# Optimization experiments

Measured on AMD Instinct MI355X. Metric: run time of the kernel, lower is better.

## Reference

```python
import jax, jax.numpy as jnp
import numpy as np

E = 256   # embed_size
H = 256   # hidden_size
C = 3     # channels
V = 257   # pixel vocab (0..255 + boundary token 256)
B, R, CO = 128, 32, 32


def setup_inputs() -> dict:
    key = jax.random.key(0)
    ks = jax.random.split(key, 16)
    s = 0.05
    return {
        "x": jax.random.randint(ks[0], (B, C, R, CO), 0, V),
        "emb": jax.random.normal(ks[1], (C, V, E), dtype=jnp.float32) * s,
        "xcomb_W": jax.random.normal(ks[2], (C, E, 2 * E), dtype=jnp.float32) * s,
        "xcomb_b": jax.random.normal(ks[3], (C, E), dtype=jnp.float32) * s,
        "hcomb_W": jax.random.normal(ks[4], (C, H, 2 * H), dtype=jnp.float32) * s,
        "hcomb_b": jax.random.normal(ks[5], (C, H), dtype=jnp.float32) * s,
        "W_ih": jax.random.normal(ks[6], (C, 3 * H, E + 2), dtype=jnp.float32) * s,
        "W_hh": jax.random.normal(ks[7], (C, 3 * H, H), dtype=jnp.float32) * s,
        "b_ih": jax.random.normal(ks[8], (C, 3 * H), dtype=jnp.float32) * s,
        "b_hh": jax.random.normal(ks[9], (C, 3 * H), dtype=jnp.float32) * s,
        "red_W": jax.random.normal(ks[10], (V, H), dtype=jnp.float32) * s,
        "red_b": jax.random.normal(ks[11], (V,), dtype=jnp.float32) * s,
        "green_W": jax.random.normal(ks[12], (V, H + E), dtype=jnp.float32) * s,
        "green_b": jax.random.normal(ks[13], (V,), dtype=jnp.float32) * s,
        "blue_W": jax.random.normal(ks[14], (V, H + 2 * E), dtype=jnp.float32) * s,
        "blue_b": jax.random.normal(ks[15], (V,), dtype=jnp.float32) * s,
    }


def _forward(x, emb, xcomb_W, xcomb_b, hcomb_W, hcomb_b, W_ih, W_hh, b_ih, b_hh,
             red_W, red_b, green_W, green_b, blue_W, blue_b):
    Bb, Cc, Rr, Co = x.shape
    Nr, Nc = Rr - 1, Co - 1
    Hd = W_hh.shape[-1]
    dt = emb.dtype

    # context pixel indices for each output position (row+1,col+1)
    left = x[:, :, 1:, :-1]    # x[:,c,row+1,col]
    above = x[:, :, :-1, 1:]   # x[:,c,row,col+1]
    target = x[:, :, 1:, 1:]   # x[:,c,row+1,col+1] (conditioning embeds for green/blue)

    # per-channel embedding gather, vectorized over all positions
    gather = jax.vmap(lambda t, idx: t[idx], in_axes=(0, 1), out_axes=1)
    left_e = gather(emb, left)      # [B,C,Nr,Nc,E]
    above_e = gather(emb, above)
    target_e = gather(emb, target)

    # x_comb linear on cat(left,above); hidden-independent -> precompute
    xi = jnp.concatenate([left_e, above_e], axis=-1)                     # [B,C,Nr,Nc,2E]
    xi = jnp.einsum('bcrke,cfe->bcrkf', xi, xcomb_W) + xcomb_b[None, :, None, None, :]

    # positional (row,col) features appended as floats (torch.cat promotion)
    pos_r = jnp.broadcast_to(jnp.arange(Nr, dtype=dt)[:, None], (Nr, Nc))
    pos_c = jnp.broadcast_to(jnp.arange(Nc, dtype=dt)[None, :], (Nr, Nc))
    pos = jnp.broadcast_to(jnp.stack([pos_r, pos_c], -1)[None, None], (Bb, Cc, Nr, Nc, 2))
    xfull = jnp.concatenate([xi, pos], axis=-1)                          # [B,C,Nr,Nc,E+2]

    # GRU input projection is hidden-independent -> precompute gates_x
    gx = jnp.einsum('bcrkf,cgf->bcrkg', xfull, W_ih) + b_ih[None, :, None, None, :]
    gx = jnp.transpose(gx, (2, 3, 1, 0, 4))                              # [Nr,Nc,C,B,3H]

    def col_step(prev_left, xs):
        gx_col, prev_row_col = xs   # [C,B,3H], [C,B,H]
        pl = prev_left              # [B,H], shared across channels and cols
        hs = []
        for c in range(Cc):         # fixed small channel loop (sequential dependence)
            hcat = jnp.concatenate([pl, prev_row_col[c]], axis=-1)       # [B,2H]
            h = hcat @ hcomb_W[c].T + hcomb_b[c]                          # [B,H]
            gh = h @ W_hh[c].T + b_hh[c]                                  # [B,3H]
            gxr, gxz, gxn = jnp.split(gx_col[c], 3, axis=-1)
            ghr, ghz, ghn = jnp.split(gh, 3, axis=-1)
            r = jax.nn.sigmoid(gxr + ghr)
            z = jax.nn.sigmoid(gxz + ghz)
            n = jnp.tanh(gxn + r * ghn)
            hnew = (1.0 - z) * n + z * h
            pl = hnew
            hs.append(hnew)
        return pl, jnp.stack(hs, 0)  # carry, [C,B,H]

    def row_step(prev_row, gx_row):
        # prev_row: hiddens from previous row [Nc,C,B,H]
        init_left = jnp.zeros((Bb, Hd), dtype=dt)
        _, hs_row = jax.lax.scan(col_step, init_left, (gx_row, prev_row))
        return hs_row, hs_row

    init_row = jnp.zeros((Nc, Cc, Bb, Hd), dtype=dt)
    _, h_all = jax.lax.scan(row_step, init_row, gx)   # [Nr,Nc,C,B,H]

    te = jnp.transpose(target_e, (2, 3, 1, 0, 4))     # [Nr,Nc,C,B,E]
    h0, h1, h2 = h_all[:, :, 0], h_all[:, :, 1], h_all[:, :, 2]  # [Nr,Nc,B,H]
    lr = h0 @ red_W.T + red_b
    lg = jnp.concatenate([h1, te[:, :, 0]], -1) @ green_W.T + green_b
    lb = jnp.concatenate([h2, te[:, :, 0], te[:, :, 1]], -1) @ blue_W.T + blue_b
    logits = jnp.stack([lr, lg, lb], 0)               # [C,Nr,Nc,B,V]
    return jnp.transpose(logits, (3, 0, 1, 2, 4))     # [B,C,Nr,Nc,V]


def reference(x, emb, xcomb_W, xcomb_b, hcomb_W, hcomb_b, W_ih, W_hh, b_ih, b_hh,
              red_W, red_b, green_W, green_b, blue_W, blue_b):
    return _forward(x, emb, xcomb_W, xcomb_b, hcomb_W, hcomb_b, W_ih, W_hh,
                    b_ih, b_hh, red_W, red_b, green_W, green_b, blue_W, blue_b)
```

## Files before the change

### kernel.cpp

```cpp
#include <hip/hip_runtime.h>

typedef __attribute__((ext_vector_type(4))) float f32x4;
typedef __attribute__((ext_vector_type(8))) short s16x8;
typedef unsigned long long u64;

__device__ __forceinline__ unsigned short f2bf(float f) {
  union { float f; unsigned u; } v; v.f = f;
  unsigned r = v.u + 0x7fffu + ((v.u >> 16) & 1u);
  return (unsigned short)(r >> 16);
}


__global__ void prep_wbig(const float* __restrict__ hcomb_W, const float* __restrict__ hcomb_b,
                          const float* __restrict__ W_hh, const float* __restrict__ b_hh,
                          unsigned short* __restrict__ Wbig, float* __restrict__ bbig) {
  __shared__ float red[256];
  const int c = blockIdx.x, g = blockIdx.y, t = threadIdx.x;
  const float* hW = hcomb_W + (size_t)c * 256 * 512;
  unsigned short* orow = Wbig + ((size_t)c * 1024 + g) * 512;
  if (g < 256) {
    orow[t]       = f2bf(hW[(size_t)g * 512 + t]);
    orow[t + 256] = f2bf(hW[(size_t)g * 512 + t + 256]);
    if (t == 0) bbig[c * 1024 + g] = hcomb_b[c * 256 + g];
    return;
  }
  const int gp = g - 256;
  const float* wrow = W_hh + ((size_t)c * 768 + gp) * 256;
  float a0 = 0.f, a1 = 0.f;
  for (int h = 0; h < 256; h++) {
    float w = wrow[h];
    a0 += w * hW[(size_t)h * 512 + t];
    a1 += w * hW[(size_t)h * 512 + t + 256];
  }
  orow[t] = f2bf(a0); orow[t + 256] = f2bf(a1);
  red[t] = wrow[t] * hcomb_b[c * 256 + t];
  __syncthreads();
  for (int s = 128; s > 0; s >>= 1) { if (t < s) red[t] += red[t + s]; __syncthreads(); }
  if (t == 0) bbig[c * 1024 + g] = red[0] + b_hh[c * 768 + gp];
}

__global__ void prep_u(const float* __restrict__ emb, const float* __restrict__ xcomb_W,
                       float* __restrict__ Ul, float* __restrict__ Ua) {
  __shared__ float er[256];
  const int c = blockIdx.x, v = blockIdx.y, side = blockIdx.z, f = threadIdx.x;
  er[f] = emb[((size_t)c * 257 + v) * 256 + f];
  __syncthreads();
  const float* wrow = xcomb_W + ((size_t)c * 256 + f) * 512 + side * 256;
  float a = 0.f;
  for (int e = 0; e < 256; e++) a += er[e] * wrow[e];
  (side ? Ua : Ul)[((size_t)c * 257 + v) * 256 + f] = a;
}

__global__ void prep_t(const float* __restrict__ W_ih, const float* __restrict__ Ul,
                       const float* __restrict__ Ua, float* __restrict__ Tl, float* __restrict__ Ta) {
  __shared__ float ur[256];
  const int c = blockIdx.x, v = blockIdx.y, side = blockIdx.z, g = threadIdx.x;
  if (g < 256) ur[g] = (side ? Ua : Ul)[((size_t)c * 257 + v) * 256 + g];
  __syncthreads();
  const float* wrow = W_ih + ((size_t)c * 768 + g) * 258;
  float a = 0.f;
  for (int f = 0; f < 256; f++) a += ur[f] * wrow[f];
  (side ? Ta : Tl)[((size_t)c * 257 + v) * 768 + g] = a;
}

__global__ void prep_bgx(const float* __restrict__ W_ih, const float* __restrict__ xcomb_b,
                         const float* __restrict__ b_ih, float* __restrict__ bgx) {
  __shared__ float xb[256];
  const int c = blockIdx.x, g = threadIdx.x;
  if (g < 256) xb[g] = xcomb_b[c * 256 + g];
  __syncthreads();
  const float* wrow = W_ih + ((size_t)c * 768 + g) * 258;
  float a = b_ih[c * 768 + g];
  for (int f = 0; f < 256; f++) a += xb[f] * wrow[f];
  bgx[c * 768 + g] = a;
}

__global__ void prep_tgb(const float* __restrict__ emb, const float* __restrict__ green_W,
                         const float* __restrict__ blue_W,
                         float* __restrict__ TG, float* __restrict__ TB0, float* __restrict__ TB1) {
  __shared__ float er[256];
  const int v = blockIdx.x, which = blockIdx.y, u = threadIdx.x;
  const int ch = (which == 2) ? 1 : 0;
  if (u < 256) er[u] = emb[((size_t)ch * 257 + v) * 256 + u];
  __syncthreads();
  if (u >= 257) return;
  const float* W; int pitch, off; float* T;
  if (which == 0)      { W = green_W; pitch = 512; off = 256; T = TG;  }
  else if (which == 1) { W = blue_W;  pitch = 768; off = 256; T = TB0; }
  else                 { W = blue_W;  pitch = 768; off = 512; T = TB1; }
  const float* wrow = W + (size_t)u * pitch + off;
  float a = 0.f;
  for (int e = 0; e < 256; e++) a += er[e] * wrow[e];
  T[(size_t)v * 257 + u] = a;
}

__global__ void prep_w3(const float* __restrict__ red_W, const float* __restrict__ green_W,
                        const float* __restrict__ blue_W, unsigned short* __restrict__ W3) {
  const int c = blockIdx.x, v = blockIdx.y, t = threadIdx.x;
  float val = 0.f;
  if (v < 257) {
    if (c == 0)      val = red_W[(size_t)v * 256 + t];
    else if (c == 1) val = green_W[(size_t)v * 512 + t];
    else             val = blue_W[(size_t)v * 768 + t];
  }
  W3[((size_t)c * 272 + v) * 256 + t] = f2bf(val);
}

__global__ void prep_gx(const int* __restrict__ x,
                        const float* __restrict__ Tl, const float* __restrict__ Ta,
                        const float* __restrict__ bgx, const float* __restrict__ bbig,
                        const float* __restrict__ W_ih, float* __restrict__ pregx) {
  __shared__ float base[768];
  __shared__ int ix0[128], ix1[128];
  const int r = blockIdx.x, k = blockIdx.y, c = blockIdx.z, tid = threadIdx.x;
  for (int g = tid; g < 768; g += 256) {
    float v = bgx[c * 768 + g]
            + (float)r * W_ih[((size_t)c * 768 + g) * 258 + 256]
            + (float)k * W_ih[((size_t)c * 768 + g) * 258 + 257];
    if (g < 512) v += bbig[c * 1024 + 256 + g];
    base[g] = v;
  }
  if (tid < 128) {
    ix0[tid] = x[((tid * 3 + c) * 32 + (r + 1)) * 32 + k];
    ix1[tid] = x[((tid * 3 + c) * 32 + r) * 32 + (k + 1)];
  }
  __syncthreads();
  const size_t cell = ((size_t)(r * 31 + k)) * 3 + c;
  float* outp = pregx + cell * 3 * 128 * 256;
  const float* Tlc = Tl + (size_t)c * 257 * 768;
  const float* Tac = Ta + (size_t)c * 257 * 768;
  #pragma unroll 2
  for (int b = 0; b < 128; ++b) {
    const float* tl = Tlc + (size_t)ix0[b] * 768;
    const float* ta = Tac + (size_t)ix1[b] * 768;
    #pragma unroll
    for (int q = 0; q < 3; ++q) {
      const int g = q * 256 + tid;
      outp[((size_t)q * 128 + b) * 256 + tid] = tl[g] + ta[g] + base[g];
    }
  }
}

__global__ void zero_flags(int* __restrict__ f, int n) {
  int i = blockIdx.x * 256 + threadIdx.x;
  if (i < n) f[i] = 0;
}


__device__ __forceinline__ void spinwait(int* f, int target) {
  while (__hip_atomic_load(f, __ATOMIC_RELAXED, __HIP_MEMORY_SCOPE_AGENT) < target)
    __builtin_amdgcn_s_sleep(2);
}

__global__ __launch_bounds__(256, 2)
void persist_kernel(const int* __restrict__ x, float* __restrict__ hbuf,
                    const unsigned short* __restrict__ Wbig, const float* __restrict__ bbig,
                    const float* __restrict__ pregx,
                    const unsigned short* __restrict__ W3,
                    const float* __restrict__ TG, const float* __restrict__ TB0,
                    const float* __restrict__ TB1,
                    const float* __restrict__ red_b, const float* __restrict__ green_b,
                    const float* __restrict__ blue_b,
                    float* __restrict__ out, int* __restrict__ flags)
{
  __shared__ unsigned short Abuf[128 * 136];
  __shared__ int idx0[128], idx1[128];

  const int id = blockIdx.x;
  const int rlo = id & 7, slot = id >> 3;
  const int rhi = slot / 5, role = slot - 5 * rhi;
  const int r = rlo + 8 * rhi;
  if (r > 30) return;

  int* sflag = flags;
  int* eflag = flags + 124 * 31;

  const int tid = threadIdx.x;
  const int lane = tid & 63, wv = tid >> 6;
  const int quad = lane >> 4, l16 = lane & 15;

  if (role < 4) {
    const int jcol = role * 64 + wv * 16;
    const int j = jcol + l16;

    for (int L = r; L <= r + 92; ++L) {
      const int t = L - r;
      const int k = t / 3, c = t - 3 * k;
      const size_t cell = ((size_t)(r * 31 + k)) * 3 + c;
      const float* pg = pregx + cell * 3 * 128 * 256;

      f32x4 acc[8][4];
      const float bh  = bbig[c * 1024 + j];
      const float bn3 = bbig[c * 1024 + 768 + j];
      #pragma unroll
      for (int mt = 0; mt < 8; ++mt)
        #pragma unroll
        for (int i = 0; i < 4; ++i) {
          const int b = mt * 16 + quad * 4 + i;
          acc[mt][0][i] = bh;
          acc[mt][1][i] = pg[(size_t)b * 256 + j];
          acc[mt][2][i] = pg[(size_t)(128 + b) * 256 + j];
          acc[mt][3][i] = bn3;
        }

      if (tid == 0) {
        if (t >= 1) spinwait(&sflag[(L - 1) * 31 + r], 4);
        if (r >= 1) spinwait(&sflag[(L - 1) * 31 + (r - 1)], 4);
        if (t >= 3) {
          if (r < 30) spinwait(&sflag[(L - 2) * 31 + (r + 1)], 4);
          spinwait(&eflag[(L - 2) * 31 + r], 1);
        }
      }
      __syncthreads();
      __builtin_amdgcn_fence(__ATOMIC_ACQUIRE, "agent");

      const bool pl_zero = (t == 0);
      const bool a_zero  = (r == 0);
      const float* plp = hbuf + ((size_t)(r * 3 + (c == 0 ? 2 : c - 1)) * 128) * 256;
      const float* ap  = (r > 0) ? hbuf + ((size_t)((r - 1) * 3 + c) * 128) * 256 : hbuf;
      const unsigned short* Wb = Wbig + (size_t)c * 1024 * 512;

      for (int kc = 0; kc < 4; ++kc) {
        const bool from_pl = (kc < 2);
        const float* src = from_pl ? plp : ap;
        const bool zero = from_pl ? pl_zero : a_zero;
        const int colbase = from_pl ? kc * 128 : (kc - 2) * 128;
        __syncthreads();
        #pragma unroll 8
        for (int it = 0; it < 16; ++it) {
          const int li = it * 256 + tid;
          const int row = li >> 5;
          const int col = (li & 31) * 4;
          unsigned short o0 = 0, o1 = 0, o2 = 0, o3 = 0;
          if (!zero) {
            const float4 v = *(const float4*)(src + (size_t)row * 256 + colbase + col);
            o0 = f2bf(v.x); o1 = f2bf(v.y); o2 = f2bf(v.z); o3 = f2bf(v.w);
          }
          unsigned short* d = &Abuf[row * 136 + col];
          d[0] = o0; d[1] = o1; d[2] = o2; d[3] = o3;
        }
        __syncthreads();
        #pragma unroll
        for (int ks = 0; ks < 4; ++ks) {
          const int kofs = ks * 32 + quad * 8;
          s16x8 bf[4];
          #pragma unroll
          for (int g = 0; g < 4; ++g)
            bf[g] = *(const s16x8*)(Wb + (size_t)(g * 256 + jcol + l16) * 512 + kc * 128 + kofs);
          #pragma unroll
          for (int mt = 0; mt < 8; ++mt) {
            const s16x8 af = *(const s16x8*)&Abuf[(mt * 16 + l16) * 136 + kofs];
            #pragma unroll
            for (int g = 0; g < 4; ++g)
              acc[mt][g] = __builtin_amdgcn_mfma_f32_16x16x32_bf16(af, bf[g], acc[mt][g], 0, 0, 0);
          }
        }
      }

      const float* pgn = pg + (size_t)2 * 128 * 256;
      float* hout = hbuf + ((size_t)(r * 3 + c) * 128) * 256;
      #pragma unroll
      for (int mt = 0; mt < 8; ++mt)
        #pragma unroll
        for (int i = 0; i < 4; ++i) {
          const int b = mt * 16 + quad * 4 + i;
          const float gxn = pgn[(size_t)b * 256 + j];
          const float h  = acc[mt][0][i];
          const float rg = __fdividef(1.f, 1.f + __expf(-acc[mt][1][i]));
          const float zg = __fdividef(1.f, 1.f + __expf(-acc[mt][2][i]));
          const float ng = 1.f - __fdividef(2.f, __expf(2.f * (gxn + rg * acc[mt][3][i])) + 1.f);
          hout[(size_t)b * 256 + j] = (1.f - zg) * ng + zg * h;
        }

      __syncthreads();
      if (tid == 0)
        __hip_atomic_fetch_add(&sflag[L * 31 + r], 1, __ATOMIC_RELEASE, __HIP_MEMORY_SCOPE_AGENT);
    }
  } else {
    for (int Le = r + 1; Le <= r + 93; ++Le) {
      const int t = Le - 1 - r;
      const int k = t / 3, c = t - 3 * k;

      if (tid == 0) spinwait(&sflag[(Le - 1) * 31 + r], 4);
      __syncthreads();
      __builtin_amdgcn_fence(__ATOMIC_ACQUIRE, "agent");

      if (tid < 128) {
        idx0[tid] = x[((tid * 3 + 0) * 32 + (r + 1)) * 32 + (k + 1)];
        idx1[tid] = x[((tid * 3 + 1) * 32 + (r + 1)) * 32 + (k + 1)];
      }

      const float* hsrc = hbuf + ((size_t)(r * 3 + c) * 128) * 256;
      const unsigned short* W3c = W3 + (size_t)c * 272 * 256;

      f32x4 acc[2][17];
      #pragma unroll
      for (int m2 = 0; m2 < 2; ++m2)
        #pragma unroll
        for (int nt = 0; nt < 17; ++nt)
          #pragma unroll
          for (int e = 0; e < 4; ++e) acc[m2][nt][e] = 0.f;

      for (int kc = 0; kc < 2; ++kc) {
        __syncthreads();
        #pragma unroll 8
        for (int it = 0; it < 16; ++it) {
          const int li = it * 256 + tid;
          const int row = li >> 5;
          const int col = (li & 31) * 4;
          const float4 v = *(const float4*)(hsrc + (size_t)row * 256 + kc * 128 + col);
          unsigned short* d = &Abuf[row * 136 + col];
          d[0] = f2bf(v.x); d[1] = f2bf(v.y); d[2] = f2bf(v.z); d[3] = f2bf(v.w);
        }
        __syncthreads();
        if (kc == 1 && tid == 0)
          __hip_atomic_fetch_add(&eflag[Le * 31 + r], 1, __ATOMIC_RELEASE, __HIP_MEMORY_SCOPE_AGENT);
        #pragma unroll
        for (int ks = 0; ks < 4; ++ks) {
          const int kofs = ks * 32 + quad * 8;
          s16x8 af[2];
          #pragma unroll
          for (int m2 = 0; m2 < 2; ++m2)
            af[m2] = *(const s16x8*)&Abuf[((wv * 2 + m2) * 16 + l16) * 136 + kofs];
          #pragma unroll
          for (int nt = 0; nt < 17; ++nt) {
            const s16x8 bf = *(const s16x8*)(W3c + (size_t)(nt * 16 + l16) * 256 + kc * 128 + kofs);
            #pragma unroll
            for (int m2 = 0; m2 < 2; ++m2)
              acc[m2][nt] = __builtin_amdgcn_mfma_f32_16x16x32_bf16(af[m2], bf, acc[m2][nt], 0, 0, 0);
          }
        }
      }

      const float* bias = (c == 0) ? red_b : (c == 1) ? green_b : blue_b;
      #pragma unroll
      for (int m2 = 0; m2 < 2; ++m2)
        #pragma unroll
        for (int i = 0; i < 4; ++i) {
          const int b = (m2 + wv * 2) * 16 + quad * 4 + i;
          const int t0 = idx0[b], t1 = idx1[b];
          float* orow = out + ((size_t)((b * 3 + c) * 31 + r) * 31 + k) * 257;
          #pragma unroll
          for (int nt = 0; nt < 17; ++nt) {
            const int v = nt * 16 + l16;
            if (v < 257) {
              float val = acc[m2][nt][i] + bias[v];
              if (c == 1)      val += TG[(size_t)t0 * 257 + v];
              else if (c == 2) val += TB0[(size_t)t0 * 257 + v] + TB1[(size_t)t1 * 257 + v];
              orow[v] = val;
            }
          }
        }
    }
  }
}


extern "C" void kernel_launch(void* const* d_in, const int* in_sizes, int n_in,
                              void* d_out, int out_size, void* d_ws, size_t ws_size,
                              hipStream_t stream) {
  const int*   x       = (const int*)  d_in[0];
  const float* emb     = (const float*)d_in[1];
  const float* xcomb_W = (const float*)d_in[2];
  const float* xcomb_b = (const float*)d_in[3];
  const float* hcomb_W = (const float*)d_in[4];
  const float* hcomb_b = (const float*)d_in[5];
  const float* W_ih    = (const float*)d_in[6];
  const float* W_hh    = (const float*)d_in[7];
  const float* b_ih    = (const float*)d_in[8];
  const float* b_hh    = (const float*)d_in[9];
  const float* red_W   = (const float*)d_in[10];
  const float* red_b   = (const float*)d_in[11];
  const float* green_W = (const float*)d_in[12];
  const float* green_b = (const float*)d_in[13];
  const float* blue_W  = (const float*)d_in[14];
  const float* blue_b  = (const float*)d_in[15];
  float* out = (float*)d_out;

  char* p = (char*)d_ws;
  auto alloc = [&](size_t bytes) -> char* {
    char* r = p; p += (bytes + 255) & ~(size_t)255; return r;
  };
  float* hbuf          = (float*)alloc((size_t)31 * 3 * 128 * 256 * 4);
  unsigned short* Wbig = (unsigned short*)alloc((size_t)3 * 1024 * 512 * 2);
  float* bbig          = (float*)alloc((size_t)3 * 1024 * 4);
  float* Tl            = (float*)alloc((size_t)3 * 257 * 768 * 4);
  float* Ta            = (float*)alloc((size_t)3 * 257 * 768 * 4);
  float* Ul            = (float*)alloc((size_t)3 * 257 * 256 * 4);
  float* Ua            = (float*)alloc((size_t)3 * 257 * 256 * 4);
  float* bgx           = (float*)alloc((size_t)3 * 768 * 4);
  unsigned short* W3   = (unsigned short*)alloc((size_t)3 * 272 * 256 * 2);
  float* TG            = (float*)alloc((size_t)257 * 257 * 4);
  float* TB0           = (float*)alloc((size_t)257 * 257 * 4);
  float* TB1           = (float*)alloc((size_t)257 * 257 * 4);
  int*   flags         = (int*)  alloc((size_t)2 * 124 * 31 * 4);
  float* pregx         = (float*)alloc((size_t)2883 * 3 * 128 * 256 * 4);

  prep_wbig<<<dim3(3, 1024), dim3(256), 0, stream>>>(hcomb_W, hcomb_b, W_hh, b_hh, Wbig, bbig);
  prep_u<<<dim3(3, 257, 2), dim3(256), 0, stream>>>(emb, xcomb_W, Ul, Ua);
  prep_t<<<dim3(3, 257, 2), dim3(768), 0, stream>>>(W_ih, Ul, Ua, Tl, Ta);
  prep_bgx<<<dim3(3), dim3(768), 0, stream>>>(W_ih, xcomb_b, b_ih, bgx);
  prep_tgb<<<dim3(257, 3), dim3(320), 0, stream>>>(emb, green_W, blue_W, TG, TB0, TB1);
  prep_w3<<<dim3(3, 272), dim3(256), 0, stream>>>(red_W, green_W, blue_W, W3);
  prep_gx<<<dim3(31, 31, 3), dim3(256), 0, stream>>>(x, Tl, Ta, bgx, bbig, W_ih, pregx);
  zero_flags<<<dim3(31), dim3(256), 0, stream>>>(flags, 2 * 124 * 31);

  persist_kernel<<<dim3(160), dim3(256), 0, stream>>>(
      x, hbuf, Wbig, bbig, pregx, W3, TG, TB0, TB1, red_b, green_b, blue_b, out, flags);
}
```

Measured before the change: 10.39 ms.

## Restructure persistent GRU kernel: one 1024-thread block per row, bf16 hidden state, fused gx

Each wavefront row now runs in a single 1024-thread block instead of four 256-thread blocks split by column. This removes the cross-block split of the recurrent GEMM, and the per-step flags need only one arrival instead of four. The precomputed combined W_hh·hcomb weight is replaced by two chained bf16 GEMMs (hcomb, then W_hh) done in double-buffered swizzled LDS. The large pregx precompute buffer is dropped, and the gate inputs are gathered from the Tl/Ta tables inside the step. Hidden state is stored as bf16 with coherent atomic loads and stores, and the logits kernel runs as 31 1024-thread blocks. The trade-off is more matmul work per step and fewer, larger blocks on the serial critical path, in exchange for cutting the large gx memory traffic and some synchronisation.

```diff
diff --git a/kernel.cpp b/kernel.cpp
--- a/kernel.cpp
+++ b/kernel.cpp
@@ -3,40 +3,26 @@
 typedef __attribute__((ext_vector_type(4))) float f32x4;
 typedef __attribute__((ext_vector_type(8))) short s16x8;
 typedef unsigned long long u64;
-
-__device__ __forceinline__ unsigned short f2bf(float f) {
+typedef unsigned short u16;
+
+__device__ __forceinline__ u16 f2bf(float f) {
   union { float f; unsigned u; } v; v.f = f;
   unsigned r = v.u + 0x7fffu + ((v.u >> 16) & 1u);
-  return (unsigned short)(r >> 16);
-}
-
-
-__global__ void prep_wbig(const float* __restrict__ hcomb_W, const float* __restrict__ hcomb_b,
-                          const float* __restrict__ W_hh, const float* __restrict__ b_hh,
-                          unsigned short* __restrict__ Wbig, float* __restrict__ bbig) {
-  __shared__ float red[256];
+  return (u16)(r >> 16);
+}
+
+
+__global__ void prep_w12(const float* __restrict__ hcomb_W, const float* __restrict__ W_hh,
+                         u16* __restrict__ W1, u16* __restrict__ W2) {
   const int c = blockIdx.x, g = blockIdx.y, t = threadIdx.x;
-  const float* hW = hcomb_W + (size_t)c * 256 * 512;
-  unsigned short* orow = Wbig + ((size_t)c * 1024 + g) * 512;
   if (g < 256) {
-    orow[t]       = f2bf(hW[(size_t)g * 512 + t]);
-    orow[t + 256] = f2bf(hW[(size_t)g * 512 + t + 256]);
-    if (t == 0) bbig[c * 1024 + g] = hcomb_b[c * 256 + g];
-    return;
+    const float* src = hcomb_W + ((size_t)c * 256 + g) * 512;
+    u16* dst = W1 + ((size_t)c * 256 + g) * 512;
+    dst[t] = f2bf(src[t]); dst[t + 256] = f2bf(src[t + 256]);
+  } else {
+    const int gp = g - 256;
+    W2[((size_t)c * 768 + gp) * 256 + t] = f2bf(W_hh[((size_t)c * 768 + gp) * 256 + t]);
   }
-  const int gp = g - 256;
-  const float* wrow = W_hh + ((size_t)c * 768 + gp) * 256;
-  float a0 = 0.f, a1 = 0.f;
-  for (int h = 0; h < 256; h++) {
-    float w = wrow[h];
-    a0 += w * hW[(size_t)h * 512 + t];
-    a1 += w * hW[(size_t)h * 512 + t + 256];
-  }
-  orow[t] = f2bf(a0); orow[t + 256] = f2bf(a1);
-  red[t] = wrow[t] * hcomb_b[c * 256 + t];
-  __syncthreads();
-  for (int s = 128; s > 0; s >>= 1) { if (t < s) red[t] += red[t + s]; __syncthreads(); }
-  if (t == 0) bbig[c * 1024 + g] = red[0] + b_hh[c * 768 + gp];
 }
 
 __global__ void prep_u(const float* __restrict__ emb, const float* __restrict__ xcomb_W,
@@ -95,7 +81,7 @@
 }
 
 __global__ void prep_w3(const float* __restrict__ red_W, const float* __restrict__ green_W,
-                        const float* __restrict__ blue_W, unsigned short* __restrict__ W3) {
+                        const float* __restrict__ blue_W, u16* __restrict__ W3) {
   const int c = blockIdx.x, v = blockIdx.y, t = threadIdx.x;
   float val = 0.f;
   if (v < 257) {
@@ -106,41 +92,6 @@
   W3[((size_t)c * 272 + v) * 256 + t] = f2bf(val);
 }
 
-__global__ void prep_gx(const int* __restrict__ x,
-                        const float* __restrict__ Tl, const float* __restrict__ Ta,
-                        const float* __restrict__ bgx, const float* __restrict__ bbig,
-                        const float* __restrict__ W_ih, float* __restrict__ pregx) {
-  __shared__ float base[768];
-  __shared__ int ix0[128], ix1[128];
-  const int r = blockIdx.x, k = blockIdx.y, c = blockIdx.z, tid = threadIdx.x;
-  for (int g = tid; g < 768; g += 256) {
-    float v = bgx[c * 768 + g]
-            + (float)r * W_ih[((size_t)c * 768 + g) * 258 + 256]
-            + (float)k * W_ih[((size_t)c * 768 + g) * 258 + 257];
-    if (g < 512) v += bbig[c * 1024 + 256 + g];
-    base[g] = v;
-  }
-  if (tid < 128) {
-    ix0[tid] = x[((tid * 3 + c) * 32 + (r + 1)) * 32 + k];
-    ix1[tid] = x[((tid * 3 + c) * 32 + r) * 32 + (k + 1)];
-  }
-  __syncthreads();
-  const size_t cell = ((size_t)(r * 31 + k)) * 3 + c;
-  float* outp = pregx + cell * 3 * 128 * 256;
-  const float* Tlc = Tl + (size_t)c * 257 * 768;
-  const float* Tac = Ta + (size_t)c * 257 * 768;
-  #pragma unroll 2
-  for (int b = 0; b < 128; ++b) {
-    const float* tl = Tlc + (size_t)ix0[b] * 768;
-    const float* ta = Tac + (size_t)ix1[b] * 768;
-    #pragma unroll
-    for (int q = 0; q < 3; ++q) {
-      const int g = q * 256 + tid;
-      outp[((size_t)q * 128 + b) * 256 + tid] = tl[g] + ta[g] + base[g];
-    }
-  }
-}
-
 __global__ void zero_flags(int* __restrict__ f, int n) {
   int i = blockIdx.x * 256 + threadIdx.x;
   if (i < n) f[i] = 0;
@@ -148,206 +99,306 @@
 
 
 __device__ __forceinline__ void spinwait(int* f, int target) {
-  while (__hip_atomic_load(f, __ATOMIC_RELAXED, __HIP_MEMORY_SCOPE_AGENT) < target)
+  for (long i = 0; i < 200000000L; ++i) {
+    if (__hip_atomic_load(f, __ATOMIC_RELAXED, __HIP_MEMORY_SCOPE_AGENT) >= target) return;
     __builtin_amdgcn_s_sleep(2);
-}
-
-__global__ __launch_bounds__(256, 2)
-void persist_kernel(const int* __restrict__ x, float* __restrict__ hbuf,
-                    const unsigned short* __restrict__ Wbig, const float* __restrict__ bbig,
-                    const float* __restrict__ pregx,
-                    const unsigned short* __restrict__ W3,
+  }
+}
+__device__ __forceinline__ u64 load_coh(const u16* p) {
+  return __hip_atomic_load((const u64*)p, __ATOMIC_RELAXED, __HIP_MEMORY_SCOPE_SYSTEM);
+}
+__device__ __forceinline__ void store_coh(u16* p, u64 v) {
+  __hip_atomic_store((u64*)p, v, __ATOMIC_RELAXED, __HIP_MEMORY_SCOPE_SYSTEM);
+}
+__device__ __forceinline__ int sw_off(int row, int el) {
+  return row * 512 + ((el * 2) ^ ((row & 7) << 4));
+}
+
+__global__ __launch_bounds__(1024, 1)
+void persist_kernel(const int* __restrict__ x, u16* __restrict__ hbuf,
+                    const u16* __restrict__ W1, const u16* __restrict__ W2,
+                    const float* __restrict__ Tl, const float* __restrict__ Ta,
+                    const float* __restrict__ bgx, const float* __restrict__ W_ih,
+                    const float* __restrict__ hcomb_b, const float* __restrict__ b_hh,
+                    const u16* __restrict__ W3,
                     const float* __restrict__ TG, const float* __restrict__ TB0,
                     const float* __restrict__ TB1,
                     const float* __restrict__ red_b, const float* __restrict__ green_b,
                     const float* __restrict__ blue_b,
                     float* __restrict__ out, int* __restrict__ flags)
 {
-  __shared__ unsigned short Abuf[128 * 136];
-  __shared__ int idx0[128], idx1[128];
-
-  const int id = blockIdx.x;
-  const int rlo = id & 7, slot = id >> 3;
-  const int rhi = slot / 5, role = slot - 5 * rhi;
-  const int r = rlo + 8 * rhi;
-  if (r > 30) return;
+  __shared__ char smem[131072];
+  __shared__ int idx0[128];
+  __shared__ int idx1[128];
 
   int* sflag = flags;
   int* eflag = flags + 124 * 31;
 
+  const int id = blockIdx.x;
   const int tid = threadIdx.x;
-  const int lane = tid & 63, wv = tid >> 6;
-  const int quad = lane >> 4, l16 = lane & 15;
-
-  if (role < 4) {
-    const int jcol = role * 64 + wv * 16;
-    const int j = jcol + l16;
+  const int w = tid >> 6, lane = tid & 63, quad = lane >> 4, l16 = lane & 15;
+
+  if (id < 31) {
+    const int r = id;
+    const int wm = w >> 3, wj = w & 7;
+    const int arow = wm * 64 + l16;
 
     for (int L = r; L <= r + 92; ++L) {
       const int t = L - r;
       const int k = t / 3, c = t - 3 * k;
-      const size_t cell = ((size_t)(r * 31 + k)) * 3 + c;
-      const float* pg = pregx + cell * 3 * 128 * 256;
-
-      f32x4 acc[8][4];
-      const float bh  = bbig[c * 1024 + j];
-      const float bn3 = bbig[c * 1024 + 768 + j];
-      #pragma unroll
-      for (int mt = 0; mt < 8; ++mt)
-        #pragma unroll
-        for (int i = 0; i < 4; ++i) {
-          const int b = mt * 16 + quad * 4 + i;
-          acc[mt][0][i] = bh;
-          acc[mt][1][i] = pg[(size_t)b * 256 + j];
-          acc[mt][2][i] = pg[(size_t)(128 + b) * 256 + j];
-          acc[mt][3][i] = bn3;
-        }
+      char* Pr = smem + ((t & 1) ? 65536 : 0);
+      char* Or = smem + ((t & 1) ? 0 : 65536);
 
       if (tid == 0) {
-        if (t >= 1) spinwait(&sflag[(L - 1) * 31 + r], 4);
-        if (r >= 1) spinwait(&sflag[(L - 1) * 31 + (r - 1)], 4);
+        if (r >= 1) spinwait(&sflag[(L - 1) * 31 + (r - 1)], 1);
         if (t >= 3) {
-          if (r < 30) spinwait(&sflag[(L - 2) * 31 + (r + 1)], 4);
+          if (r < 30) spinwait(&sflag[(L - 2) * 31 + (r + 1)], 1);
           spinwait(&eflag[(L - 2) * 31 + r], 1);
         }
       }
       __syncthreads();
-      __builtin_amdgcn_fence(__ATOMIC_ACQUIRE, "agent");
+      __builtin_amdgcn_fence(__ATOMIC_ACQUIRE, "workgroup");
 
       const bool pl_zero = (t == 0);
       const bool a_zero  = (r == 0);
-      const float* plp = hbuf + ((size_t)(r * 3 + (c == 0 ? 2 : c - 1)) * 128) * 256;
-      const float* ap  = (r > 0) ? hbuf + ((size_t)((r - 1) * 3 + c) * 128) * 256 : hbuf;
-      const unsigned short* Wb = Wbig + (size_t)c * 1024 * 512;
-
-      for (int kc = 0; kc < 4; ++kc) {
-        const bool from_pl = (kc < 2);
-        const float* src = from_pl ? plp : ap;
-        const bool zero = from_pl ? pl_zero : a_zero;
-        const int colbase = from_pl ? kc * 128 : (kc - 2) * 128;
-        __syncthreads();
-        #pragma unroll 8
-        for (int it = 0; it < 16; ++it) {
-          const int li = it * 256 + tid;
-          const int row = li >> 5;
-          const int col = (li & 31) * 4;
-          unsigned short o0 = 0, o1 = 0, o2 = 0, o3 = 0;
-          if (!zero) {
-            const float4 v = *(const float4*)(src + (size_t)row * 256 + colbase + col);
-            o0 = f2bf(v.x); o1 = f2bf(v.y); o2 = f2bf(v.z); o3 = f2bf(v.w);
-          }
-          unsigned short* d = &Abuf[row * 136 + col];
-          d[0] = o0; d[1] = o1; d[2] = o2; d[3] = o3;
-        }
-        __syncthreads();
-        #pragma unroll
-        for (int ks = 0; ks < 4; ++ks) {
-          const int kofs = ks * 32 + quad * 8;
-          s16x8 bf[4];
-          #pragma unroll
-          for (int g = 0; g < 4; ++g)
-            bf[g] = *(const s16x8*)(Wb + (size_t)(g * 256 + jcol + l16) * 512 + kc * 128 + kofs);
-          #pragma unroll
-          for (int mt = 0; mt < 8; ++mt) {
-            const s16x8 af = *(const s16x8*)&Abuf[(mt * 16 + l16) * 136 + kofs];
-            #pragma unroll
-            for (int g = 0; g < 4; ++g)
-              acc[mt][g] = __builtin_amdgcn_mfma_f32_16x16x32_bf16(af, bf[g], acc[mt][g], 0, 0, 0);
-          }
-        }
-      }
-
-      const float* pgn = pg + (size_t)2 * 128 * 256;
-      float* hout = hbuf + ((size_t)(r * 3 + c) * 128) * 256;
-      #pragma unroll
-      for (int mt = 0; mt < 8; ++mt)
-        #pragma unroll
-        for (int i = 0; i < 4; ++i) {
-          const int b = mt * 16 + quad * 4 + i;
-          const float gxn = pgn[(size_t)b * 256 + j];
-          const float h  = acc[mt][0][i];
-          const float rg = __fdividef(1.f, 1.f + __expf(-acc[mt][1][i]));
-          const float zg = __fdividef(1.f, 1.f + __expf(-acc[mt][2][i]));
-          const float ng = 1.f - __fdividef(2.f, __expf(2.f * (gxn + rg * acc[mt][3][i])) + 1.f);
-          hout[(size_t)b * 256 + j] = (1.f - zg) * ng + zg * h;
-        }
-
+
+      u64 sa0[4], sa1[4];
+      if (!a_zero) {
+        const u16* hgA = hbuf + (size_t)((r - 1) * 3 + c) * 32768;
+        #pragma unroll
+        for (int q = 0; q < 4; ++q) {
+          const int ch = q * 1024 + tid, row = ch >> 5, cs = ch & 31;
+          const u16* sp = hgA + row * 256 + cs * 8;
+          sa0[q] = load_coh(sp); sa1[q] = load_coh(sp + 4);
+        }
+      }
+      if (tid < 128) {
+        idx0[tid] = x[((tid * 3 + c) * 32 + (r + 1)) * 32 + k];
+        idx1[tid] = x[((tid * 3 + c) * 32 + r) * 32 + (k + 1)];
+      }
+
+      const u16* W1c = W1 + (size_t)c * 256 * 512;
+      f32x4 acc1[4][2];
+      #pragma unroll
+      for (int mi = 0; mi < 4; ++mi)
+        #pragma unroll
+        for (int ji = 0; ji < 2; ++ji)
+          #pragma unroll
+          for (int e = 0; e < 4; ++e) acc1[mi][ji][e] = 0.f;
+
+      if (!pl_zero) {
+        #pragma unroll
+        for (int kc = 0; kc < 2; ++kc)
+          #pragma unroll
+          for (int ks = 0; ks < 4; ++ks) {
+            const int kof = kc * 128 + ks * 32 + quad * 8;
+            s16x8 bf[2];
+            #pragma unroll
+            for (int ji = 0; ji < 2; ++ji)
+              bf[ji] = *(const s16x8*)(W1c + (size_t)(ji * 128 + wj * 16 + l16) * 512 + kof);
+            #pragma unroll
+            for (int mi = 0; mi < 4; ++mi) {
+              const s16x8 af = *(const s16x8*)(Pr + sw_off(arow + mi * 16, kof));
+              #pragma unroll
+              for (int ji = 0; ji < 2; ++ji)
+                acc1[mi][ji] = __builtin_amdgcn_mfma_f32_16x16x32_bf16(af, bf[ji], acc1[mi][ji], 0, 0, 0);
+            }
+          }
+      }
+      if (!a_zero) {
+        #pragma unroll
+        for (int q = 0; q < 4; ++q) {
+          const int ch = q * 1024 + tid, row = ch >> 5, cs = ch & 31;
+          const int s = sw_off(row, cs * 8);
+          *(u64*)(Or + s) = sa0[q]; *(u64*)(Or + s + 8) = sa1[q];
+        }
+      }
+      __syncthreads();
+
+      if (!a_zero) {
+        #pragma unroll
+        for (int kc = 0; kc < 2; ++kc)
+          #pragma unroll
+          for (int ks = 0; ks < 4; ++ks) {
+            const int ke = kc * 128 + ks * 32 + quad * 8;
+            s16x8 bf[2];
+            #pragma unroll
+            for (int ji = 0; ji < 2; ++ji)
+              bf[ji] = *(const s16x8*)(W1c + (size_t)(ji * 128 + wj * 16 + l16) * 512 + 256 + ke);
+            #pragma unroll
+            for (int mi = 0; mi < 4; ++mi) {
+              const s16x8 af = *(const s16x8*)(Or + sw_off(arow + mi * 16, ke));
+              #pragma unroll
+              for (int ji = 0; ji < 2; ++ji)
+                acc1[mi][ji] = __builtin_amdgcn_mfma_f32_16x16x32_bf16(af, bf[ji], acc1[mi][ji], 0, 0, 0);
+            }
+          }
+      }
+      #pragma unroll
+      for (int ji = 0; ji < 2; ++ji) {
+        const int j = ji * 128 + wj * 16 + l16;
+        const float bh = hcomb_b[c * 256 + j];
+        #pragma unroll
+        for (int mi = 0; mi < 4; ++mi)
+          #pragma unroll
+          for (int ii = 0; ii < 4; ++ii) {
+            const int b = (wm * 4 + mi) * 16 + quad * 4 + ii;
+            *(u16*)(Pr + sw_off(b, j)) = f2bf(acc1[mi][ji][ii] + bh);
+          }
+      }
+      __syncthreads();
+
+      const u16* W2c = W2 + (size_t)c * 768 * 256;
+      const float* Tlc = Tl + (size_t)c * 257 * 768;
+      const float* Tac = Ta + (size_t)c * 257 * 768;
+      const float fr = (float)r, fk = (float)k;
+
+      #pragma unroll
+      for (int jh = 0; jh < 2; ++jh) {
+        const int j2 = jh * 128 + wj * 16 + l16;
+        float gx0[3], bh3[3];
+        #pragma unroll
+        for (int q = 0; q < 3; ++q) {
+          const int gi = c * 768 + q * 256 + j2;
+          gx0[q] = bgx[gi] + fr * W_ih[(size_t)gi * 258 + 256] + fk * W_ih[(size_t)gi * 258 + 257];
+          bh3[q] = b_hh[gi];
+        }
+        const float bh2 = hcomb_b[c * 256 + j2];
+
+        f32x4 acc2[4][3];
+        float gxn[4][4];
+        #pragma unroll
+        for (int mi = 0; mi < 4; ++mi)
+          #pragma unroll
+          for (int ii = 0; ii < 4; ++ii) {
+            const int b = (wm * 4 + mi) * 16 + quad * 4 + ii;
+            const float* tl = Tlc + (size_t)idx0[b] * 768 + j2;
+            const float* ta = Tac + (size_t)idx1[b] * 768 + j2;
+            acc2[mi][0][ii] = gx0[0] + tl[0]   + ta[0]   + bh3[0];
+            acc2[mi][1][ii] = gx0[1] + tl[256] + ta[256] + bh3[1];
+            acc2[mi][2][ii] = bh3[2];
+            gxn[mi][ii]     = gx0[2] + tl[512] + ta[512];
+          }
+
+        #pragma unroll
+        for (int ks = 0; ks < 8; ++ks) {
+          const int kof = ks * 32 + quad * 8;
+          s16x8 bf[3];
+          #pragma unroll
+          for (int q = 0; q < 3; ++q)
+            bf[q] = *(const s16x8*)(W2c + (size_t)(q * 256 + j2) * 256 + kof);
+          #pragma unroll
+          for (int mi = 0; mi < 4; ++mi) {
+            const s16x8 af = *(const s16x8*)(Pr + sw_off(arow + mi * 16, kof));
+            #pragma unroll
+            for (int q = 0; q < 3; ++q)
+              acc2[mi][q] = __builtin_amdgcn_mfma_f32_16x16x32_bf16(af, bf[q], acc2[mi][q], 0, 0, 0);
+          }
+        }
+
+        #pragma unroll
+        for (int mi = 0; mi < 4; ++mi)
+          #pragma unroll
+          for (int ii = 0; ii < 4; ++ii) {
+            const int b = (wm * 4 + mi) * 16 + quad * 4 + ii;
+            const float h  = acc1[mi][jh][ii] + bh2;
+            const float rg = __fdividef(1.f, 1.f + __expf(-acc2[mi][0][ii]));
+            const float zg = __fdividef(1.f, 1.f + __expf(-acc2[mi][1][ii]));
+            const float ng = 1.f - __fdividef(2.f,
+                __expf(2.f * (gxn[mi][ii] + rg * acc2[mi][2][ii])) + 1.f);
+            *(u16*)(Or + sw_off(b, j2)) = f2bf((1.f - zg) * ng + zg * h);
+          }
+      }
+      __syncthreads();
+
+      u16* hgW = hbuf + (size_t)(r * 3 + c) * 32768;
+      #pragma unroll
+      for (int q = 0; q < 4; ++q) {
+        const int ch = q * 1024 + tid, row = ch >> 5, cs = ch & 31;
+        const int s = sw_off(row, cs * 8);
+        store_coh(hgW + row * 256 + cs * 8,     *(const u64*)(Or + s));
+        store_coh(hgW + row * 256 + cs * 8 + 4, *(const u64*)(Or + s + 8));
+      }
       __syncthreads();
       if (tid == 0)
-        __hip_atomic_fetch_add(&sflag[L * 31 + r], 1, __ATOMIC_RELEASE, __HIP_MEMORY_SCOPE_AGENT);
+        __hip_atomic_fetch_add(&sflag[L * 31 + r], 1, __ATOMIC_RELAXED, __HIP_MEMORY_SCOPE_AGENT);
     }
   } else {
+    const int r = id - 31;
+    const int wmE = w & 3, wnE = w >> 2;
+    const int NT = wnE ? 4 : 5;
+    const int nbase = wnE ? (1 + wnE * 4) : 0;
+
     for (int Le = r + 1; Le <= r + 93; ++Le) {
       const int t = Le - 1 - r;
       const int k = t / 3, c = t - 3 * k;
 
-      if (tid == 0) spinwait(&sflag[(Le - 1) * 31 + r], 4);
-      __syncthreads();
-      __builtin_amdgcn_fence(__ATOMIC_ACQUIRE, "agent");
-
+      if (tid == 0) spinwait(&sflag[(Le - 1) * 31 + r], 1);
+      __syncthreads();
+      __builtin_amdgcn_fence(__ATOMIC_ACQUIRE, "workgroup");
+
+      const u16* hgS = hbuf + (size_t)(r * 3 + c) * 32768;
+      #pragma unroll
+      for (int q = 0; q < 4; ++q) {
+        const int ch = q * 1024 + tid, row = ch >> 5, cs = ch & 31;
+        const u16* sp = hgS + row * 256 + cs * 8;
+        const u64 a0 = load_coh(sp), a1 = load_coh(sp + 4);
+        const int s = sw_off(row, cs * 8);
+        *(u64*)(smem + s) = a0; *(u64*)(smem + s + 8) = a1;
+      }
       if (tid < 128) {
         idx0[tid] = x[((tid * 3 + 0) * 32 + (r + 1)) * 32 + (k + 1)];
         idx1[tid] = x[((tid * 3 + 1) * 32 + (r + 1)) * 32 + (k + 1)];
       }
-
-      const float* hsrc = hbuf + ((size_t)(r * 3 + c) * 128) * 256;
-      const unsigned short* W3c = W3 + (size_t)c * 272 * 256;
-
-      f32x4 acc[2][17];
-      #pragma unroll
-      for (int m2 = 0; m2 < 2; ++m2)
-        #pragma unroll
-        for (int nt = 0; nt < 17; ++nt)
-          #pragma unroll
-          for (int e = 0; e < 4; ++e) acc[m2][nt][e] = 0.f;
-
-      for (int kc = 0; kc < 2; ++kc) {
-        __syncthreads();
-        #pragma unroll 8
-        for (int it = 0; it < 16; ++it) {
-          const int li = it * 256 + tid;
-          const int row = li >> 5;
-          const int col = (li & 31) * 4;
-          const float4 v = *(const float4*)(hsrc + (size_t)row * 256 + kc * 128 + col);
-          unsigned short* d = &Abuf[row * 136 + col];
-          d[0] = f2bf(v.x); d[1] = f2bf(v.y); d[2] = f2bf(v.z); d[3] = f2bf(v.w);
-        }
-        __syncthreads();
-        if (kc == 1 && tid == 0)
-          __hip_atomic_fetch_add(&eflag[Le * 31 + r], 1, __ATOMIC_RELEASE, __HIP_MEMORY_SCOPE_AGENT);
-        #pragma unroll
-        for (int ks = 0; ks < 4; ++ks) {
-          const int kofs = ks * 32 + quad * 8;
-          s16x8 af[2];
-          #pragma unroll
-          for (int m2 = 0; m2 < 2; ++m2)
-            af[m2] = *(const s16x8*)&Abuf[((wv * 2 + m2) * 16 + l16) * 136 + kofs];
-          #pragma unroll
-          for (int nt = 0; nt < 17; ++nt) {
-            const s16x8 bf = *(const s16x8*)(W3c + (size_t)(nt * 16 + l16) * 256 + kc * 128 + kofs);
-            #pragma unroll
-            for (int m2 = 0; m2 < 2; ++m2)
-              acc[m2][nt] = __builtin_amdgcn_mfma_f32_16x16x32_bf16(af[m2], bf, acc[m2][nt], 0, 0, 0);
+      __syncthreads();
+      if (tid == 0)
+        __hip_atomic_fetch_add(&eflag[Le * 31 + r], 1, __ATOMIC_RELAXED, __HIP_MEMORY_SCOPE_AGENT);
+
+      const u16* W3c = W3 + (size_t)c * 272 * 256;
+      f32x4 acc[2][5];
+      #pragma unroll
+      for (int mi = 0; mi < 2; ++mi)
+        #pragma unroll
+        for (int ni = 0; ni < 5; ++ni)
+          #pragma unroll
+          for (int e = 0; e < 4; ++e) acc[mi][ni][e] = 0.f;
+
+      #pragma unroll
+      for (int ks = 0; ks < 8; ++ks) {
+        const int kof = ks * 32 + quad * 8;
+        s16x8 af[2];
+        #pragma unroll
+        for (int mi = 0; mi < 2; ++mi)
+          af[mi] = *(const s16x8*)(smem + sw_off((wmE * 2 + mi) * 16 + l16, kof));
+        #pragma unroll
+        for (int ni = 0; ni < 5; ++ni) {
+          if (ni < NT) {
+            const s16x8 bf = *(const s16x8*)(W3c + (size_t)((nbase + ni) * 16 + l16) * 256 + kof);
+            #pragma unroll
+            for (int mi = 0; mi < 2; ++mi)
+              acc[mi][ni] = __builtin_amdgcn_mfma_f32_16x16x32_bf16(af[mi], bf, acc[mi][ni], 0, 0, 0);
           }
         }
       }
 
       const float* bias = (c == 0) ? red_b : (c == 1) ? green_b : blue_b;
       #pragma unroll
-      for (int m2 = 0; m2 < 2; ++m2)
-        #pragma unroll
-        for (int i = 0; i < 4; ++i) {
-          const int b = (m2 + wv * 2) * 16 + quad * 4 + i;
+      for (int mi = 0; mi < 2; ++mi)
+        #pragma unroll
+        for (int ii = 0; ii < 4; ++ii) {
+          const int b = (wmE * 2 + mi) * 16 + quad * 4 + ii;
           const int t0 = idx0[b], t1 = idx1[b];
           float* orow = out + ((size_t)((b * 3 + c) * 31 + r) * 31 + k) * 257;
           #pragma unroll
-          for (int nt = 0; nt < 17; ++nt) {
-            const int v = nt * 16 + l16;
-            if (v < 257) {
-              float val = acc[m2][nt][i] + bias[v];
-              if (c == 1)      val += TG[(size_t)t0 * 257 + v];
-              else if (c == 2) val += TB0[(size_t)t0 * 257 + v] + TB1[(size_t)t1 * 257 + v];
-              orow[v] = val;
+          for (int ni = 0; ni < 5; ++ni) {
+            if (ni < NT) {
+              const int v = (nbase + ni) * 16 + l16;
+              if (v < 257) {
+                float val = acc[mi][ni][ii] + bias[v];
+                if (c == 1)      val += TG[(size_t)t0 * 257 + v];
+                else if (c == 2) val += TB0[(size_t)t0 * 257 + v] + TB1[(size_t)t1 * 257 + v];
+                orow[v] = val;
+              }
             }
           }
         }
@@ -381,30 +432,29 @@
   auto alloc = [&](size_t bytes) -> char* {
     char* r = p; p += (bytes + 255) & ~(size_t)255; return r;
   };
-  float* hbuf          = (float*)alloc((size_t)31 * 3 * 128 * 256 * 4);
-  unsigned short* Wbig = (unsigned short*)alloc((size_t)3 * 1024 * 512 * 2);
-  float* bbig          = (float*)alloc((size_t)3 * 1024 * 4);
-  float* Tl            = (float*)alloc((size_t)3 * 257 * 768 * 4);
-  float* Ta            = (float*)alloc((size_t)3 * 257 * 768 * 4);
-  float* Ul            = (float*)alloc((size_t)3 * 257 * 256 * 4);
-  float* Ua            = (float*)alloc((size_t)3 * 257 * 256 * 4);
-  float* bgx           = (float*)alloc((size_t)3 * 768 * 4);
-  unsigned short* W3   = (unsigned short*)alloc((size_t)3 * 272 * 256 * 2);
-  float* TG            = (float*)alloc((size_t)257 * 257 * 4);
-  float* TB0           = (float*)alloc((size_t)257 * 257 * 4);
-  float* TB1           = (float*)alloc((size_t)257 * 257 * 4);
-  int*   flags         = (int*)  alloc((size_t)2 * 124 * 31 * 4);
-  float* pregx         = (float*)alloc((size_t)2883 * 3 * 128 * 256 * 4);
-
-  prep_wbig<<<dim3(3, 1024), dim3(256), 0, stream>>>(hcomb_W, hcomb_b, W_hh, b_hh, Wbig, bbig);
+  u16*   hbuf  = (u16*)  alloc((size_t)93 * 128 * 256 * 2);
+  u16*   W1    = (u16*)  alloc((size_t)3 * 256 * 512 * 2);
+  u16*   W2    = (u16*)  alloc((size_t)3 * 768 * 256 * 2);
+  float* Tl    = (float*)alloc((size_t)3 * 257 * 768 * 4);
+  float* Ta    = (float*)alloc((size_t)3 * 257 * 768 * 4);
+  float* Ul    = (float*)alloc((size_t)3 * 257 * 256 * 4);
+  float* Ua    = (float*)alloc((size_t)3 * 257 * 256 * 4);
+  float* bgx   = (float*)alloc((size_t)3 * 768 * 4);
+  u16*   W3    = (u16*)  alloc((size_t)3 * 272 * 256 * 2);
+  float* TG    = (float*)alloc((size_t)257 * 257 * 4);
+  float* TB0   = (float*)alloc((size_t)257 * 257 * 4);
+  float* TB1   = (float*)alloc((size_t)257 * 257 * 4);
+  int*   flags = (int*)  alloc((size_t)2 * 124 * 31 * 4);
+
+  prep_w12<<<dim3(3, 1024), dim3(256), 0, stream>>>(hcomb_W, W_hh, W1, W2);
   prep_u<<<dim3(3, 257, 2), dim3(256), 0, stream>>>(emb, xcomb_W, Ul, Ua);
   prep_t<<<dim3(3, 257, 2), dim3(768), 0, stream>>>(W_ih, Ul, Ua, Tl, Ta);
   prep_bgx<<<dim3(3), dim3(768), 0, stream>>>(W_ih, xcomb_b, b_ih, bgx);
   prep_tgb<<<dim3(257, 3), dim3(320), 0, stream>>>(emb, green_W, blue_W, TG, TB0, TB1);
   prep_w3<<<dim3(3, 272), dim3(256), 0, stream>>>(red_W, green_W, blue_W, W3);
-  prep_gx<<<dim3(31, 31, 3), dim3(256), 0, stream>>>(x, Tl, Ta, bgx, bbig, W_ih, pregx);
   zero_flags<<<dim3(31), dim3(256), 0, stream>>>(flags, 2 * 124 * 31);
 
-  persist_kernel<<<dim3(160), dim3(256), 0, stream>>>(
-      x, hbuf, Wbig, bbig, pregx, W3, TG, TB0, TB1, red_b, green_b, blue_b, out, flags);
-}
+  persist_kernel<<<dim3(62), dim3(1024), 0, stream>>>(
+      x, hbuf, W1, W2, Tl, Ta, bgx, W_ih, hcomb_b, b_hh, W3, TG, TB0, TB1,
+      red_b, green_b, blue_b, out, flags);
+}
```

Result: slower. 12.25 ms (+17.9%).
